# Optimization experiments

Measured on AMD Instinct MI355X. Metric: run time of the kernel, lower is better.

The kernel has to match this reference:

```python
import jax, jax.numpy as jnp
import numpy as np

B, N, M = 8192, 4096, 256


def setup_inputs() -> dict:
    key = jax.random.key(0)
    k_x, k_keep, k_w1, k_b1, k_w2, k_b2 = jax.random.split(key, 6)
    x = jax.random.normal(k_x, (B, N), dtype=jnp.float32)
    keep = jax.random.uniform(k_keep, (B, N)) < 0.5
    x = jnp.where(keep, x, 0.0)
    # Linear params, PyTorch-style fan-in scaling
    W1 = jax.random.normal(k_w1, (N, M), dtype=jnp.float32) / np.sqrt(N)
    b1 = jax.random.normal(k_b1, (M,), dtype=jnp.float32) * 0.01
    W2 = jax.random.normal(k_w2, (M, N), dtype=jnp.float32) / np.sqrt(M)
    b2 = jax.random.normal(k_b2, (N,), dtype=jnp.float32) * 0.01
    return {"x": x, "W1": W1, "b1": b1, "W2": W2, "b2": b2}


def reference(x, W1, b1, W2, b2):
    # f2(relu(f1(x)))
    f = jax.nn.relu(x @ W1 + b1) @ W2 + b2  # [B, N]
    mask = x != 0
    # per-row sum over masked positions (vectorized version of the Python loop)
    s = jnp.sum(jnp.where(mask, f, 0.0), axis=1, keepdims=True)  # [B, 1]
    # rows with empty mask stay all-zero; guard divide-by-zero for those rows
    s_safe = jnp.where(s == 0.0, 1.0, s)
    y = jnp.where(mask, f / s_safe, 0.0)
    return y
```

## Files before the change

### kernel.cpp

```cpp
#include <hip/hip_runtime.h>

typedef _Float16 f16;
typedef _Float16 f16x8 __attribute__((ext_vector_type(8)));
typedef float f32x4 __attribute__((ext_vector_type(4)));

#define MFMA16(a,b,c) __builtin_amdgcn_mfma_f32_16x16x32_f16((a),(b),(c),0,0,0)

__device__ __forceinline__ void gload16(const void* g, void* l) {
  __builtin_amdgcn_global_load_lds(
      (const __attribute__((address_space(1))) void*)g,
      (__attribute__((address_space(3))) void*)l, 16, 0, 0);
}

__device__ __forceinline__ int swz(int r, int c) {
  return r * 32 + ((c ^ (r & 3)) << 3);
}

__device__ __forceinline__ void split8n(const f32x4 v0, const f32x4 v1,
                                        f16x8& hv, f16x8& lv) {
#pragma unroll
  for (int j = 0; j < 4; ++j) {
    f16 h0 = (f16)v0[j]; hv[j] = h0; lv[j] = (f16)(v0[j] - (float)h0);
    f16 h1 = (f16)v1[j]; hv[j + 4] = h1; lv[j + 4] = (f16)(v1[j] - (float)h1);
  }
}

__global__ __launch_bounds__(256) void k_prep(const float* __restrict__ in,
                                              f16* __restrict__ oh, f16* __restrict__ ol,
                                              int R, int C, int trShift) {
  __shared__ float t[64][65];
  int c0 = blockIdx.x * 64, r0 = blockIdx.y * 64;
  int tid = threadIdx.x;
#pragma unroll
  for (int i = 0; i < 16; ++i) {
    int idx = tid + i * 256;
    int r = idx >> 6, c = idx & 63;
    t[r][c] = in[(size_t)(r0 + r) * C + (c0 + c)];
  }
  __syncthreads();
  int ktiles = R >> 5;
  int TRm1 = (1 << trShift) - 1;
#pragma unroll
  for (int w = 0; w < 2; ++w) {
    int idx = tid + w * 256;
    int nn = idx >> 3, cc8 = idx & 7;
    f32x4 v0, v1;
#pragma unroll
    for (int j = 0; j < 4; ++j) v0[j] = t[cc8 * 8 + j][nn];
#pragma unroll
    for (int j = 0; j < 4; ++j) v1[j] = t[cc8 * 8 + 4 + j][nn];
    f16x8 hv, lv;
    split8n(v0, v1, hv, lv);
    int gn = c0 + nn, gk = r0 + cc8 * 8;
    size_t tileIdx = (size_t)(gn >> trShift) * ktiles + (gk >> 5);
    size_t off = (tileIdx << (trShift + 5)) + ((size_t)(gn & TRm1) << 5) +
                 (((cc8 & 3) ^ (gn & 3)) << 3);
    *(f16x8*)&oh[off] = hv;
    *(f16x8*)&ol[off] = lv;
  }
}

__global__ __launch_bounds__(128, 2) void k_g1(
    const float* __restrict__ X, const f16* __restrict__ Bht,
    const f16* __restrict__ Blt, unsigned char* __restrict__ mb,
    float* __restrict__ partials) {
  __shared__ f16 smB[3][8192];
  int bx = blockIdx.x, nb = blockIdx.y, kc = blockIdx.z;
  int tid = threadIdx.x;
  int wid = tid >> 6, ln = tid & 63, lr = ln & 15, lg = ln >> 4;
  const int NS = 16;
  int m0 = bx * 128, kb0 = kc * 512;
  size_t bt0 = ((size_t)nb * 128 + (size_t)kc * 16) * 4096;
  bool domask = (nb == 0);

  const float* xb = X + (size_t)(m0 + wid * 64 + lr) * 4096 + kb0 + lg * 8;
  const size_t XF = (size_t)16 * 4096;

  f32x4 areg[8];
  f16x8 ah[4], al[4];
  f32x4 acc[4][8] = {};

  auto issueA = [&](int s) {
#pragma unroll
    for (int fi = 0; fi < 4; ++fi) {
      const float* p = xb + (size_t)fi * XF + s * 32;
      areg[fi * 2] = *(const f32x4*)p;
      areg[fi * 2 + 1] = *(const f32x4*)(p + 4);
    }
  };
  auto stageB = [&](int s, int buf) {
    const f16* bh = Bht + bt0 + (size_t)s * 4096;
    const f16* bl = Blt + bt0 + (size_t)s * 4096;
#pragma unroll
    for (int i = 0; i < 4; ++i)
      gload16(bh + ((i * 2 + wid) * 512 + ln * 8), &smB[buf][(i * 2 + wid) * 512]);
#pragma unroll
    for (int i = 0; i < 4; ++i)
      gload16(bl + ((i * 2 + wid) * 512 + ln * 8),
              &smB[buf][4096 + (i * 2 + wid) * 512]);
  };
  auto splitA = [&](int s) {
#pragma unroll
    for (int fi = 0; fi < 4; ++fi)
      split8n(areg[fi * 2], areg[fi * 2 + 1], ah[fi], al[fi]);
    if (domask) {
#pragma unroll
      for (int fi = 0; fi < 4; ++fi) {
        unsigned m = 0;
#pragma unroll
        for (int j = 0; j < 4; ++j) {
          if (areg[fi * 2][j] != 0.f) m |= 1u << j;
          if (areg[fi * 2 + 1][j] != 0.f) m |= 1u << (4 + j);
        }
        int row = m0 + wid * 64 + fi * 16 + lr;
        int gk = kb0 + s * 32 + lg * 8;
        mb[(size_t)row * 512 + (gk >> 3)] = (unsigned char)m;
      }
    }
  };

  issueA(0);
  stageB(0, 0);
  stageB(1, 1);
  asm volatile("s_waitcnt vmcnt(8)" ::: "memory");
  __builtin_amdgcn_sched_barrier(0);
  splitA(0);
  __builtin_amdgcn_s_barrier();

  int cb = 0;
  for (int s = 0; s < NS; ++s) {
    bool moreA = (s + 1) < NS;
    bool moreB = (s + 2) < NS;
    if (moreA) issueA(s + 1);
    if (moreB) {
      int pb = cb + 2; if (pb >= 3) pb -= 3;
      stageB(s + 2, pb);
    }
#pragma unroll
    for (int g = 0; g < 2; ++g) {
      f16x8 fbh[4], fbl[4];
#pragma unroll
      for (int j = 0; j < 4; ++j) {
        int c = (g * 4 + j) * 16 + lr;
        fbh[j] = *(const f16x8*)&smB[cb][swz(c, lg)];
        fbl[j] = *(const f16x8*)&smB[cb][4096 + swz(c, lg)];
      }
#pragma unroll
      for (int fi = 0; fi < 4; ++fi)
#pragma unroll
        for (int j = 0; j < 4; ++j) {
          acc[fi][g * 4 + j] = MFMA16(ah[fi], fbh[j], acc[fi][g * 4 + j]);
          acc[fi][g * 4 + j] = MFMA16(ah[fi], fbl[j], acc[fi][g * 4 + j]);
          acc[fi][g * 4 + j] = MFMA16(al[fi], fbh[j], acc[fi][g * 4 + j]);
        }
    }
    if (s + 1 < NS) {
      if (moreB)
        asm volatile("s_waitcnt vmcnt(8)" ::: "memory");
      else
        asm volatile("s_waitcnt vmcnt(0)" ::: "memory");
      __builtin_amdgcn_sched_barrier(0);
      splitA(s + 1);
      __builtin_amdgcn_s_barrier();
    }
    cb = cb + 1; if (cb >= 3) cb -= 3;
  }

  float* pout = partials + (size_t)kc * 8192 * 256;
#pragma unroll
  for (int fi = 0; fi < 4; ++fi)
#pragma unroll
    for (int fj = 0; fj < 8; ++fj)
#pragma unroll
      for (int q = 0; q < 4; ++q) {
        int row = m0 + wid * 64 + fi * 16 + lg * 4 + q;
        int col = nb * 128 + fj * 16 + lr;
        pout[(size_t)row * 256 + col] = acc[fi][fj][q];
      }
}

__global__ __launch_bounds__(256) void k_hsplit(const float* __restrict__ p,
                                                const float* __restrict__ b1,
                                                f16* __restrict__ Hh,
                                                f16* __restrict__ Hl) {
  int g = blockIdx.x * 256 + threadIdx.x;
  int r = g >> 5, c = g & 31;
  const size_t CH = (size_t)8192 * 256;
  const float* p0 = p + (size_t)r * 256 + c * 8;
  f32x4 s0 = *(const f32x4*)p0, s1 = *(const f32x4*)(p0 + 4);
#pragma unroll
  for (int q = 1; q < 8; ++q) {
    f32x4 d0 = *(const f32x4*)(p0 + q * CH), d1 = *(const f32x4*)(p0 + q * CH + 4);
#pragma unroll
    for (int j = 0; j < 4; ++j) { s0[j] += d0[j]; s1[j] += d1[j]; }
  }
  f32x4 bb0 = *(const f32x4*)(b1 + c * 8), bb1 = *(const f32x4*)(b1 + c * 8 + 4);
  f32x4 v0, v1;
#pragma unroll
  for (int j = 0; j < 4; ++j) {
    float v = s0[j] + bb0[j];
    v0[j] = v > 0.f ? v : 0.f;
    float w = s1[j] + bb1[j];
    v1[j] = w > 0.f ? w : 0.f;
  }
  f16x8 hv, lv;
  split8n(v0, v1, hv, lv);
  size_t tileIdx = (size_t)(r >> 7) * 8 + (c >> 2);
  size_t off = tileIdx * 4096 + ((size_t)(r & 127) << 5) + (((c & 3) ^ (r & 3)) << 3);
  *(f16x8*)&Hh[off] = hv;
  *(f16x8*)&Hl[off] = lv;
}

__global__ __launch_bounds__(256, 2) void k_gemm2b(
    const f16* __restrict__ At_h, const f16* __restrict__ At_l,
    const f16* __restrict__ Bt_h, const f16* __restrict__ Bt_l,
    const float* __restrict__ b2, const unsigned* __restrict__ maskw,
    f16* __restrict__ fout, float* __restrict__ partials) {
  __shared__ f16 smA[2][2][4096];
  __shared__ f16 smB[2][2][4096];
  __shared__ unsigned mlds[128][4];
  __shared__ float rsum[128][2];
  int bx = blockIdx.x, by = blockIdx.y;
  int m0 = bx * 128, n0 = by * 128;
  int tid = threadIdx.x;
  int wv = tid >> 6, ln = tid & 63, lr = ln & 15, lg = ln >> 4;
  int wr = wv >> 1, wc = wv & 1;
#pragma unroll
  for (int i = 0; i < 2; ++i) {
    int idx = tid + i * 256;
    mlds[idx >> 2][idx & 3] =
        maskw[(size_t)(m0 + (idx >> 2)) * 128 + by * 4 + (idx & 3)];
  }
  size_t at0 = (size_t)bx * 8 * 4096;
  size_t bt0 = (size_t)by * 8 * 4096;

  auto stage = [&](int s, int buf) {
#pragma unroll
    for (int w = 0; w < 2; ++w) {
      size_t o = (size_t)(w * 4 + wv) * 512 + (size_t)ln * 8;
      gload16(At_h + at0 + (size_t)s * 4096 + o, &smA[buf][0][(w * 4 + wv) * 512]);
      gload16(At_l + at0 + (size_t)s * 4096 + o, &smA[buf][1][(w * 4 + wv) * 512]);
      gload16(Bt_h + bt0 + (size_t)s * 4096 + o, &smB[buf][0][(w * 4 + wv) * 512]);
      gload16(Bt_l + bt0 + (size_t)s * 4096 + o, &smB[buf][1][(w * 4 + wv) * 512]);
    }
  };

  f32x4 acc[4][4] = {};
  stage(0, 0);
  __syncthreads();
  int cur = 0;
  for (int s = 0; s < 8; ++s) {
    if (s + 1 < 8) stage(s + 1, cur ^ 1);
    f16x8 fah[4], fal[4], fbh[4], fbl[4];
#pragma unroll
    for (int f = 0; f < 4; ++f) {
      int r = wr * 64 + f * 16 + lr;
      fah[f] = *(const f16x8*)&smA[cur][0][swz(r, lg)];
      fal[f] = *(const f16x8*)&smA[cur][1][swz(r, lg)];
      int c = wc * 64 + f * 16 + lr;
      fbh[f] = *(const f16x8*)&smB[cur][0][swz(c, lg)];
      fbl[f] = *(const f16x8*)&smB[cur][1][swz(c, lg)];
    }
#pragma unroll
    for (int fi = 0; fi < 4; ++fi)
#pragma unroll
      for (int fj = 0; fj < 4; ++fj) {
        acc[fi][fj] = MFMA16(fah[fi], fbh[fj], acc[fi][fj]);
        acc[fi][fj] = MFMA16(fah[fi], fbl[fj], acc[fi][fj]);
        acc[fi][fj] = MFMA16(fal[fi], fbh[fj], acc[fi][fj]);
      }
    __syncthreads();
    cur ^= 1;
  }

  float rp[4][4] = {};
#pragma unroll
  for (int fi = 0; fi < 4; ++fi)
#pragma unroll
    for (int fj = 0; fj < 4; ++fj)
#pragma unroll
      for (int q = 0; q < 4; ++q) {
        int row = wr * 64 + fi * 16 + lg * 4 + q;
        int col = wc * 64 + fj * 16 + lr;
        float v = acc[fi][fj][q] + b2[n0 + col];
        unsigned wd = mlds[row][col >> 5];
        float mv = ((wd >> (col & 31)) & 1u) ? v : 0.f;
        fout[(size_t)(m0 + row) * 4096 + (n0 + col)] = (f16)mv;
        rp[fi][q] += mv;
      }
#pragma unroll
  for (int fi = 0; fi < 4; ++fi)
#pragma unroll
    for (int q = 0; q < 4; ++q) {
      float sv = rp[fi][q];
      sv += __shfl_xor(sv, 1);
      sv += __shfl_xor(sv, 2);
      sv += __shfl_xor(sv, 4);
      sv += __shfl_xor(sv, 8);
      if (lr == 0) rsum[wr * 64 + fi * 16 + lg * 4 + q][wc] = sv;
    }
  __syncthreads();
  if (tid < 128)
    partials[(size_t)(m0 + tid) * 32 + by] = rsum[tid][0] + rsum[tid][1];
}

__global__ __launch_bounds__(256) void k_rowinv(const float* __restrict__ partials,
                                                float* __restrict__ inv) {
  int r = blockIdx.x * 256 + threadIdx.x;
  if (r < 8192) {
    float s = 0.f;
#pragma unroll 4
    for (int i = 0; i < 32; ++i) s += partials[(size_t)r * 32 + i];
    float ss = (s == 0.f) ? 1.f : s;
    inv[r] = 1.f / ss;
  }
}

__global__ __launch_bounds__(256) void k_scale16(const f16* __restrict__ f,
                                                 const float* __restrict__ inv,
                                                 float* __restrict__ out) {
  int v = blockIdx.x * 256 + threadIdx.x;
  float iv = inv[v >> 9];
  f16x8 d = *(const f16x8*)(f + (size_t)v * 8);
  f32x4 o0, o1;
#pragma unroll
  for (int j = 0; j < 4; ++j) {
    o0[j] = (float)d[j] * iv;
    o1[j] = (float)d[4 + j] * iv;
  }
  *(f32x4*)(out + (size_t)v * 8) = o0;
  *(f32x4*)(out + (size_t)v * 8 + 4) = o1;
}

extern "C" void kernel_launch(void* const* d_in, const int* in_sizes, int n_in,
                              void* d_out, int out_size, void* d_ws, size_t ws_size,
                              hipStream_t stream) {
  const float* x  = (const float*)d_in[0];
  const float* W1 = (const float*)d_in[1];
  const float* b1 = (const float*)d_in[2];
  const float* W2 = (const float*)d_in[3];
  const float* b2 = (const float*)d_in[4];
  float* out = (float*)d_out;
  char* ws = (char*)d_ws;

  const size_t MB = (size_t)1 << 20;
  f16* W1t_h = (f16*)(ws + 0 * MB);
  f16* W1t_l = (f16*)(ws + 2 * MB);
  f16* W2t_h = (f16*)(ws + 4 * MB);
  f16* W2t_l = (f16*)(ws + 6 * MB);
  f16* Hh    = (f16*)(ws + 8 * MB);
  f16* Hl    = (f16*)(ws + 12 * MB);
  unsigned char* mb = (unsigned char*)(ws + 16 * MB);
  float* part1 = (float*)(ws + 20 * MB);
  float* part2 = (float*)(ws + 84 * MB);
  float* inv_s = (float*)(ws + 85 * MB);
  f16* fbuf    = (f16*)(ws + 86 * MB);

  k_prep<<<dim3(4, 64), 256, 0, stream>>>(W1, W1t_h, W1t_l, 4096, 256, 7);
  k_prep<<<dim3(64, 4), 256, 0, stream>>>(W2, W2t_h, W2t_l, 256, 4096, 7);
  k_g1<<<dim3(64, 2, 8), 128, 0, stream>>>(x, W1t_h, W1t_l, mb, part1);
  k_hsplit<<<1024, 256, 0, stream>>>(part1, b1, Hh, Hl);
  k_gemm2b<<<dim3(64, 32), 256, 0, stream>>>(Hh, Hl, W2t_h, W2t_l, b2,
                                             (const unsigned*)mb, fbuf, part2);
  k_rowinv<<<32, 256, 0, stream>>>(part2, inv_s);
  k_scale16<<<16384, 256, 0, stream>>>(fbuf, inv_s, out);
}
```

Before: 230.4 us.

## Split k_g1 block into four waves in a 2x2 warp tile

The first GEMM kernel now runs four waves per block instead of two. Each wave computes a 64x64 sub-tile (rows by wr, columns by wc) instead of 64x128, which halves the accumulators per wave. The B-tile staging is spread across four waves and the vmcnt waits are adjusted to match. This raises the number of waves available to hide latency and lowers register pressure. In exchange, each pair of waves sharing a row loads the same A rows from global memory, so A traffic and the float-to-f16 split work are duplicated, and the mask bytes are written twice.

```diff
diff --git a/kernel.cpp b/kernel.cpp
--- a/kernel.cpp
+++ b/kernel.cpp
@@ -60,25 +60,26 @@
   }
 }
 
-__global__ __launch_bounds__(128, 2) void k_g1(
+__global__ __launch_bounds__(256, 2) void k_g1(
     const float* __restrict__ X, const f16* __restrict__ Bht,
     const f16* __restrict__ Blt, unsigned char* __restrict__ mb,
     float* __restrict__ partials) {
   __shared__ f16 smB[3][8192];
   int bx = blockIdx.x, nb = blockIdx.y, kc = blockIdx.z;
   int tid = threadIdx.x;
-  int wid = tid >> 6, ln = tid & 63, lr = ln & 15, lg = ln >> 4;
+  int wv = tid >> 6, ln = tid & 63, lr = ln & 15, lg = ln >> 4;
+  int wr = wv >> 1, wc = wv & 1;
   const int NS = 16;
   int m0 = bx * 128, kb0 = kc * 512;
   size_t bt0 = ((size_t)nb * 128 + (size_t)kc * 16) * 4096;
   bool domask = (nb == 0);
 
-  const float* xb = X + (size_t)(m0 + wid * 64 + lr) * 4096 + kb0 + lg * 8;
+  const float* xb = X + (size_t)(m0 + wr * 64 + lr) * 4096 + kb0 + lg * 8;
   const size_t XF = (size_t)16 * 4096;
 
   f32x4 areg[8];
   f16x8 ah[4], al[4];
-  f32x4 acc[4][8] = {};
+  f32x4 acc[4][4] = {};
 
   auto issueA = [&](int s) {
 #pragma unroll
@@ -92,12 +93,12 @@
     const f16* bh = Bht + bt0 + (size_t)s * 4096;
     const f16* bl = Blt + bt0 + (size_t)s * 4096;
 #pragma unroll
-    for (int i = 0; i < 4; ++i)
-      gload16(bh + ((i * 2 + wid) * 512 + ln * 8), &smB[buf][(i * 2 + wid) * 512]);
-#pragma unroll
-    for (int i = 0; i < 4; ++i)
-      gload16(bl + ((i * 2 + wid) * 512 + ln * 8),
-              &smB[buf][4096 + (i * 2 + wid) * 512]);
+    for (int i = 0; i < 2; ++i)
+      gload16(bh + ((i * 4 + wv) * 512 + ln * 8), &smB[buf][(i * 4 + wv) * 512]);
+#pragma unroll
+    for (int i = 0; i < 2; ++i)
+      gload16(bl + ((i * 4 + wv) * 512 + ln * 8),
+              &smB[buf][4096 + (i * 4 + wv) * 512]);
   };
   auto splitA = [&](int s) {
 #pragma unroll
@@ -112,7 +113,7 @@
           if (areg[fi * 2][j] != 0.f) m |= 1u << j;
           if (areg[fi * 2 + 1][j] != 0.f) m |= 1u << (4 + j);
         }
-        int row = m0 + wid * 64 + fi * 16 + lr;
+        int row = m0 + wr * 64 + fi * 16 + lr;
         int gk = kb0 + s * 32 + lg * 8;
         mb[(size_t)row * 512 + (gk >> 3)] = (unsigned char)m;
       }
@@ -122,7 +123,7 @@
   issueA(0);
   stageB(0, 0);
   stageB(1, 1);
-  asm volatile("s_waitcnt vmcnt(8)" ::: "memory");
+  asm volatile("s_waitcnt vmcnt(4)" ::: "memory");
   __builtin_amdgcn_sched_barrier(0);
   splitA(0);
   __builtin_amdgcn_s_barrier();
@@ -136,27 +137,24 @@
       int pb = cb + 2; if (pb >= 3) pb -= 3;
       stageB(s + 2, pb);
     }
-#pragma unroll
-    for (int g = 0; g < 2; ++g) {
-      f16x8 fbh[4], fbl[4];
-#pragma unroll
-      for (int j = 0; j < 4; ++j) {
-        int c = (g * 4 + j) * 16 + lr;
-        fbh[j] = *(const f16x8*)&smB[cb][swz(c, lg)];
-        fbl[j] = *(const f16x8*)&smB[cb][4096 + swz(c, lg)];
-      }
-#pragma unroll
-      for (int fi = 0; fi < 4; ++fi)
-#pragma unroll
-        for (int j = 0; j < 4; ++j) {
-          acc[fi][g * 4 + j] = MFMA16(ah[fi], fbh[j], acc[fi][g * 4 + j]);
-          acc[fi][g * 4 + j] = MFMA16(ah[fi], fbl[j], acc[fi][g * 4 + j]);
-          acc[fi][g * 4 + j] = MFMA16(al[fi], fbh[j], acc[fi][g * 4 + j]);
-        }
-    }
-    if (s + 1 < NS) {
+    f16x8 fbh[4], fbl[4];
+#pragma unroll
+    for (int fj = 0; fj < 4; ++fj) {
+      int c = wc * 64 + fj * 16 + lr;
+      fbh[fj] = *(const f16x8*)&smB[cb][swz(c, lg)];
+      fbl[fj] = *(const f16x8*)&smB[cb][4096 + swz(c, lg)];
+    }
+#pragma unroll
+    for (int fi = 0; fi < 4; ++fi)
+#pragma unroll
+      for (int fj = 0; fj < 4; ++fj) {
+        acc[fi][fj] = MFMA16(ah[fi], fbh[fj], acc[fi][fj]);
+        acc[fi][fj] = MFMA16(ah[fi], fbl[fj], acc[fi][fj]);
+        acc[fi][fj] = MFMA16(al[fi], fbh[fj], acc[fi][fj]);
+      }
+    if (moreA) {
       if (moreB)
-        asm volatile("s_waitcnt vmcnt(8)" ::: "memory");
+        asm volatile("s_waitcnt vmcnt(4)" ::: "memory");
       else
         asm volatile("s_waitcnt vmcnt(0)" ::: "memory");
       __builtin_amdgcn_sched_barrier(0);
@@ -170,11 +168,11 @@
 #pragma unroll
   for (int fi = 0; fi < 4; ++fi)
 #pragma unroll
-    for (int fj = 0; fj < 8; ++fj)
+    for (int fj = 0; fj < 4; ++fj)
 #pragma unroll
       for (int q = 0; q < 4; ++q) {
-        int row = m0 + wid * 64 + fi * 16 + lg * 4 + q;
-        int col = nb * 128 + fj * 16 + lr;
+        int row = m0 + wr * 64 + fi * 16 + lg * 4 + q;
+        int col = nb * 128 + wc * 64 + fj * 16 + lr;
         pout[(size_t)row * 256 + col] = acc[fi][fj][q];
       }
 }
@@ -358,7 +356,7 @@
 
   k_prep<<<dim3(4, 64), 256, 0, stream>>>(W1, W1t_h, W1t_l, 4096, 256, 7);
   k_prep<<<dim3(64, 4), 256, 0, stream>>>(W2, W2t_h, W2t_l, 256, 4096, 7);
-  k_g1<<<dim3(64, 2, 8), 128, 0, stream>>>(x, W1t_h, W1t_l, mb, part1);
+  k_g1<<<dim3(64, 2, 8), 256, 0, stream>>>(x, W1t_h, W1t_l, mb, part1);
   k_hsplit<<<1024, 256, 0, stream>>>(part1, b1, Hh, Hl);
   k_gemm2b<<<dim3(64, 32), 256, 0, stream>>>(Hh, Hl, W2t_h, W2t_l, b2,
                                              (const unsigned*)mb, fbuf, part2);
```

Result: slower. 252.5 us (+9.6%).
